# Kernel optimization log

Measured on AMD Instinct MI355X. Metric: run time of the kernel, lower is better.

The kernel has to match this reference:

```python
import jax, jax.numpy as jnp
import numpy as np
import math

PHI = (1.0 + math.sqrt(5.0)) / 2.0
LUT_N = 4096
_TWO_PI = 2.0 * math.pi
_ang = np.arange(LUT_N, dtype=np.float32) * (_TWO_PI / LUT_N)
SIN_T = jnp.asarray(np.sin(_ang), dtype=jnp.float32)
COS_T = jnp.asarray(np.cos(_ang), dtype=jnp.float32)


def lookup_sin_cos(theta):
    # Linearly-interpolated 4096-entry sin/cos LUT over [0, 2pi)
    pos = theta * (LUT_N / _TWO_PI)
    i0f = jnp.floor(pos)
    frac = pos - i0f
    i0 = i0f.astype(jnp.int32) % LUT_N
    i1 = (i0 + 1) % LUT_N
    sin = SIN_T[i0] * (1.0 - frac) + SIN_T[i1] * frac
    cos = COS_T[i0] * (1.0 - frac) + COS_T[i1] * frac
    return sin, cos


def setup_inputs() -> dict:
    key = jax.random.key(0)
    ks = jax.random.split(key, 10)
    B, D, H = 8192, 1024, 4
    dh = D // H
    return {
        "x_real": jax.random.normal(ks[0], (B, D), dtype=jnp.float32),
        "x_imag": jax.random.normal(ks[1], (B, D), dtype=jnp.float32),
        "t": jax.random.uniform(ks[2], (B,), dtype=jnp.float32) * 100.0,
        "trigger_real": jax.random.normal(ks[3], (H, dh), dtype=jnp.float32) * 0.5,
        "trigger_imag": jax.random.normal(ks[4], (H, dh), dtype=jnp.float32) * 0.5,
        "w_query": jax.random.normal(ks[5], (H, dh), dtype=jnp.float32) * 0.02,
        "b_query": jnp.zeros((H, dh), dtype=jnp.float32),
        "w_out": jax.random.normal(ks[6], (D,), dtype=jnp.float32) * 0.02,
        "b_out": jnp.zeros((D,), dtype=jnp.float32),
        "beta": jnp.abs(jax.random.normal(ks[7], (D,), dtype=jnp.float32)) * 5.0 + 5.0,
    }


def reference(x_real, x_imag, t, trigger_real, trigger_imag, w_query, b_query,
              w_out, b_out, beta):
    B, D = x_real.shape
    H, dh = trigger_real.shape
    t_phi = (t * PHI)[:, None]            # (B, 1)

    # ---- per-head conjugate interference ----
    xr = x_real.reshape(B, H, dh)
    xi = x_imag.reshape(B, H, dh)
    wl_q = 1.0 + jnp.abs(w_query)          # (H, dh)
    tp = t_phi[:, :, None]                 # (B, 1, 1)
    th_r = xr / wl_q + b_query + tp        # (B, H, dh)
    th_i = xi / wl_q + b_query + tp
    sin_r, cos_r = lookup_sin_cos(th_r)
    sin_i, cos_i = lookup_sin_cos(th_i)
    q_r = cos_r * cos_i - sin_r * sin_i
    q_i = cos_r * sin_i + sin_r * cos_i
    int_r = (q_r * trigger_real + q_i * trigger_imag).sum(-1)   # (B, H)
    int_i = (q_r * trigger_imag - q_i * trigger_real).sum(-1)   # (B, H)
    tot_r = int_r.mean(-1)                 # (B,)
    tot_i = int_i.mean(-1)
    mag = jnp.sqrt(tot_r * tot_r + tot_i * tot_i + 1e-8)[:, None]  # (B, 1)

    # ---- gated Q-EMA memory update (memory starts at zeros) ----
    beta_eff = 1.0 / (1.0 + jnp.abs(beta))     # (D,)
    w_eff = 1.0 / (1.0 + jnp.abs(w_out))       # (D,)
    decay = jnp.minimum(jnp.exp(-beta_eff * w_eff), 0.9999)
    write_scale = w_eff * (1.0 - decay)        # (D,)
    # initial memory is zero, so memory*decay term vanishes
    mem_r = x_real * mag * write_scale
    mem_i = x_imag * mag * write_scale

    # ---- Euler output projection ----
    wl_out = 1.0 + jnp.abs(w_out)
    to_r = mem_r / wl_out + b_out + t_phi
    to_i = mem_i / wl_out + b_out + t_phi
    s_or, c_or = lookup_sin_cos(to_r)
    s_oi, c_oi = lookup_sin_cos(to_i)
    out_real = c_or * c_oi - s_or * s_oi
    out_imag = c_or * s_oi + s_or * c_oi
    return out_real, out_imag
```

## Files before the change

kernel.cpp:

```cpp
#include <hip/hip_runtime.h>
#include <math.h>

#define DCOLS 1024
#define PHI_F 1.61803398874989484820f

__global__ __launch_bounds__(256) void echo_kernel(
    const float* __restrict__ x_real,
    const float* __restrict__ x_imag,
    const float* __restrict__ t,
    const float* __restrict__ trig_r,
    const float* __restrict__ trig_i,
    const float* __restrict__ w_query,
    const float* __restrict__ b_query,
    const float* __restrict__ w_out,
    const float* __restrict__ b_out,
    const float* __restrict__ beta,
    float* __restrict__ out_real,
    float* __restrict__ out_imag)
{
    const int b   = blockIdx.x;
    const int tid = threadIdx.x;
    const int d0  = tid << 2;
    const long base = (long)b * DCOLS + d0;

    const float tphi2 = 2.0f * PHI_F * t[b];

    float4 xr = *reinterpret_cast<const float4*>(x_real + base);
    float4 xi = *reinterpret_cast<const float4*>(x_imag + base);
    float4 wq = *reinterpret_cast<const float4*>(w_query + d0);
    float4 bq = *reinterpret_cast<const float4*>(b_query + d0);
    float4 tr = *reinterpret_cast<const float4*>(trig_r  + d0);
    float4 ti = *reinterpret_cast<const float4*>(trig_i  + d0);

    float s_sum[4];
    float tot_r = 0.f, tot_i = 0.f;
    #pragma unroll
    for (int k = 0; k < 4; ++k) {
        const float xrk = (&xr.x)[k], xik = (&xi.x)[k];
        const float s = xrk + xik;
        s_sum[k] = s;
        const float inv_wlq = __builtin_amdgcn_rcpf(1.0f + fabsf((&wq.x)[k]));
        const float ang = fmaf(s, inv_wlq, 2.0f * (&bq.x)[k] + tphi2);
        float sn, cs;
        __sincosf(ang, &sn, &cs);
        const float trk = (&tr.x)[k], tik = (&ti.x)[k];
        tot_r = fmaf(cs, trk, fmaf(sn, tik, tot_r));
        tot_i = fmaf(cs, tik, fmaf(-sn, trk, tot_i));
    }

    #pragma unroll
    for (int m = 32; m >= 1; m >>= 1) {
        tot_r += __shfl_xor(tot_r, m, 64);
        tot_i += __shfl_xor(tot_i, m, 64);
    }
    __shared__ float red_r[4], red_i[4];
    const int wid = tid >> 6;
    if ((tid & 63) == 0) { red_r[wid] = tot_r; red_i[wid] = tot_i; }
    __syncthreads();
    float TR = ((red_r[0] + red_r[1]) + (red_r[2] + red_r[3])) * 0.25f;
    float TI = ((red_i[0] + red_i[1]) + (red_i[2] + red_i[3])) * 0.25f;
    const float mag = sqrtf(fmaf(TR, TR, fmaf(TI, TI, 1e-8f)));

    float4 wo = *reinterpret_cast<const float4*>(w_out + d0);
    float4 bo = *reinterpret_cast<const float4*>(b_out + d0);
    float4 be = *reinterpret_cast<const float4*>(beta  + d0);

    float4 o_r, o_i;
    #pragma unroll
    for (int k = 0; k < 4; ++k) {
        const float weff = __builtin_amdgcn_rcpf(1.0f + fabsf((&wo.x)[k]));
        const float beff = __builtin_amdgcn_rcpf(1.0f + fabsf((&be.x)[k]));
        const float decay = fminf(__expf(-beff * weff), 0.9999f);
        const float wscale = weff * (1.0f - decay);
        const float ang = fmaf(s_sum[k], mag * wscale * weff,
                               2.0f * (&bo.x)[k] + tphi2);
        float sn, cs;
        __sincosf(ang, &sn, &cs);
        (&o_r.x)[k] = cs;
        (&o_i.x)[k] = sn;
    }
    *reinterpret_cast<float4*>(out_real + base) = o_r;
    *reinterpret_cast<float4*>(out_imag + base) = o_i;
}

extern "C" void kernel_launch(void* const* d_in, const int* in_sizes, int n_in,
                              void* d_out, int out_size, void* d_ws, size_t ws_size,
                              hipStream_t stream) {
    const float* x_real = (const float*)d_in[0];
    const float* x_imag = (const float*)d_in[1];
    const float* t      = (const float*)d_in[2];
    const float* trig_r = (const float*)d_in[3];
    const float* trig_i = (const float*)d_in[4];
    const float* w_q    = (const float*)d_in[5];
    const float* b_q    = (const float*)d_in[6];
    const float* w_out  = (const float*)d_in[7];
    const float* b_out  = (const float*)d_in[8];
    const float* beta   = (const float*)d_in[9];

    const int B = in_sizes[2];
    float* out_real = (float*)d_out;
    float* out_imag = (float*)d_out + (long)B * DCOLS;

    echo_kernel<<<B, 256, 0, stream>>>(x_real, x_imag, t,
                                       trig_r, trig_i, w_q, b_q,
                                       w_out, b_out, beta,
                                       out_real, out_imag);
}
```

Measured before the change: 141.5 us.

## Process one row per wave persistently with register-cached params and prefetch

Switches from one 256-thread block per row to one wavefront per row. Each wave loops over rows spaced total_waves apart and prefetches the next row's x and t while it computes the current one. Per-column parameters, including decay and write scale, are computed once per thread and kept in registers, which removes the shared-memory reduction, the __syncthreads, and the repeated parameter work. In exchange the kernel uses more registers (launch bounds 256,2) and launches fewer blocks (B/16 blocks, so each wave handles 4 rows), which may limit latency hiding.

```diff
diff --git a/kernel.cpp b/kernel.cpp
--- a/kernel.cpp
+++ b/kernel.cpp
@@ -4,83 +4,123 @@
 #define DCOLS 1024
 #define PHI_F 1.61803398874989484820f
 
-__global__ __launch_bounds__(256) void echo_kernel(
-    const float* __restrict__ x_real,
-    const float* __restrict__ x_imag,
+__global__ __launch_bounds__(256, 2) void echo_kernel(
+    const float* __restrict__ x_real, const float* __restrict__ x_imag,
     const float* __restrict__ t,
-    const float* __restrict__ trig_r,
-    const float* __restrict__ trig_i,
-    const float* __restrict__ w_query,
-    const float* __restrict__ b_query,
-    const float* __restrict__ w_out,
-    const float* __restrict__ b_out,
+    const float* __restrict__ trig_r, const float* __restrict__ trig_i,
+    const float* __restrict__ w_query, const float* __restrict__ b_query,
+    const float* __restrict__ w_out, const float* __restrict__ b_out,
     const float* __restrict__ beta,
-    float* __restrict__ out_real,
-    float* __restrict__ out_imag)
+    float* __restrict__ out_real, float* __restrict__ out_imag,
+    int B, int total_waves)
 {
-    const int b   = blockIdx.x;
-    const int tid = threadIdx.x;
-    const int d0  = tid << 2;
-    const long base = (long)b * DCOLS + d0;
+    const int tid  = threadIdx.x;
+    const int lane = tid & 63;
+    const int wid  = tid >> 6;
+    const int wave = (blockIdx.x << 2) + wid;
+    const int c0   = lane << 2;
 
-    const float tphi2 = 2.0f * PHI_F * t[b];
-
-    float4 xr = *reinterpret_cast<const float4*>(x_real + base);
-    float4 xi = *reinterpret_cast<const float4*>(x_imag + base);
-    float4 wq = *reinterpret_cast<const float4*>(w_query + d0);
-    float4 bq = *reinterpret_cast<const float4*>(b_query + d0);
-    float4 tr = *reinterpret_cast<const float4*>(trig_r  + d0);
-    float4 ti = *reinterpret_cast<const float4*>(trig_i  + d0);
-
-    float s_sum[4];
-    float tot_r = 0.f, tot_i = 0.f;
+    float invq[16], addq[16], trr[16], tri[16], c2[16], addo[16];
     #pragma unroll
     for (int k = 0; k < 4; ++k) {
-        const float xrk = (&xr.x)[k], xik = (&xi.x)[k];
-        const float s = xrk + xik;
-        s_sum[k] = s;
-        const float inv_wlq = __builtin_amdgcn_rcpf(1.0f + fabsf((&wq.x)[k]));
-        const float ang = fmaf(s, inv_wlq, 2.0f * (&bq.x)[k] + tphi2);
-        float sn, cs;
-        __sincosf(ang, &sn, &cs);
-        const float trk = (&tr.x)[k], tik = (&ti.x)[k];
-        tot_r = fmaf(cs, trk, fmaf(sn, tik, tot_r));
-        tot_i = fmaf(cs, tik, fmaf(-sn, trk, tot_i));
+        const int c = (k << 8) + c0;
+        const float4 wq = *reinterpret_cast<const float4*>(w_query + c);
+        const float4 bq = *reinterpret_cast<const float4*>(b_query + c);
+        const float4 tr = *reinterpret_cast<const float4*>(trig_r  + c);
+        const float4 ti = *reinterpret_cast<const float4*>(trig_i  + c);
+        const float4 wo = *reinterpret_cast<const float4*>(w_out   + c);
+        const float4 bo = *reinterpret_cast<const float4*>(b_out   + c);
+        const float4 be = *reinterpret_cast<const float4*>(beta    + c);
+        #pragma unroll
+        for (int j = 0; j < 4; ++j) {
+            const int e = (k << 2) + j;
+            invq[e] = __builtin_amdgcn_rcpf(1.0f + fabsf((&wq.x)[j]));
+            addq[e] = 2.0f * (&bq.x)[j];
+            trr[e]  = (&tr.x)[j];
+            tri[e]  = (&ti.x)[j];
+            const float weff  = __builtin_amdgcn_rcpf(1.0f + fabsf((&wo.x)[j]));
+            const float beff  = __builtin_amdgcn_rcpf(1.0f + fabsf((&be.x)[j]));
+            const float decay = fminf(__expf(-beff * weff), 0.9999f);
+            c2[e]   = weff * weff * (1.0f - decay);
+            addo[e] = 2.0f * (&bo.x)[j];
+        }
     }
 
-    #pragma unroll
-    for (int m = 32; m >= 1; m >>= 1) {
-        tot_r += __shfl_xor(tot_r, m, 64);
-        tot_i += __shfl_xor(tot_i, m, 64);
-    }
-    __shared__ float red_r[4], red_i[4];
-    const int wid = tid >> 6;
-    if ((tid & 63) == 0) { red_r[wid] = tot_r; red_i[wid] = tot_i; }
-    __syncthreads();
-    float TR = ((red_r[0] + red_r[1]) + (red_r[2] + red_r[3])) * 0.25f;
-    float TI = ((red_i[0] + red_i[1]) + (red_i[2] + red_i[3])) * 0.25f;
-    const float mag = sqrtf(fmaf(TR, TR, fmaf(TI, TI, 1e-8f)));
+    int row = wave;
+    if (row >= B) return;
+    long base = (long)row * DCOLS + c0;
 
-    float4 wo = *reinterpret_cast<const float4*>(w_out + d0);
-    float4 bo = *reinterpret_cast<const float4*>(b_out + d0);
-    float4 be = *reinterpret_cast<const float4*>(beta  + d0);
-
-    float4 o_r, o_i;
+    float4 xr[4], xi[4];
     #pragma unroll
     for (int k = 0; k < 4; ++k) {
-        const float weff = __builtin_amdgcn_rcpf(1.0f + fabsf((&wo.x)[k]));
-        const float beff = __builtin_amdgcn_rcpf(1.0f + fabsf((&be.x)[k]));
-        const float decay = fminf(__expf(-beff * weff), 0.9999f);
-        const float wscale = weff * (1.0f - decay);
-        const float ang = fmaf(s_sum[k], mag * wscale * weff,
-                               2.0f * (&bo.x)[k] + tphi2);
-        float sn, cs;
-        __sincosf(ang, &sn, &cs);
-        (&o_r.x)[k] = cs;
-        (&o_i.x)[k] = sn;
+        xr[k] = *reinterpret_cast<const float4*>(x_real + base + (k << 8));
+        xi[k] = *reinterpret_cast<const float4*>(x_imag + base + (k << 8));
     }
-    *reinterpret_cast<float4*>(out_real + base) = o_r;
-    *reinterpret_cast<float4*>(out_imag + base) = o_i;
+    float tcur = t[row];
+
+    while (true) {
+        const int  nrow = row + total_waves;
+        const bool more = (nrow < B);
+        const float tphi2 = 2.0f * PHI_F * tcur;
+
+        float s[16];
+        float tot_r = 0.f, tot_i = 0.f;
+        #pragma unroll
+        for (int k = 0; k < 4; ++k) {
+            #pragma unroll
+            for (int j = 0; j < 4; ++j) {
+                const int e = (k << 2) + j;
+                const float sv = (&xr[k].x)[j] + (&xi[k].x)[j];
+                s[e] = sv;
+                const float ang = fmaf(sv, invq[e], addq[e] + tphi2);
+                float sn, cs;
+                __sincosf(ang, &sn, &cs);
+                tot_r = fmaf(cs, trr[e], fmaf(sn, tri[e], tot_r));
+                tot_i = fmaf(cs, tri[e], fmaf(-sn, trr[e], tot_i));
+            }
+        }
+
+        float4 nxr[4], nxi[4];
+        float tnext = 0.f;
+        const long nbase = (long)nrow * DCOLS + c0;
+        if (more) {
+            #pragma unroll
+            for (int k = 0; k < 4; ++k) {
+                nxr[k] = *reinterpret_cast<const float4*>(x_real + nbase + (k << 8));
+                nxi[k] = *reinterpret_cast<const float4*>(x_imag + nbase + (k << 8));
+            }
+            tnext = t[nrow];
+        }
+
+        #pragma unroll
+        for (int m = 32; m >= 1; m >>= 1) {
+            tot_r += __shfl_xor(tot_r, m, 64);
+            tot_i += __shfl_xor(tot_i, m, 64);
+        }
+        const float TR = tot_r * 0.25f, TI = tot_i * 0.25f;
+        const float mag = sqrtf(fmaf(TR, TR, fmaf(TI, TI, 1e-8f)));
+
+        #pragma unroll
+        for (int k = 0; k < 4; ++k) {
+            float4 o_r, o_i;
+            #pragma unroll
+            for (int j = 0; j < 4; ++j) {
+                const int e = (k << 2) + j;
+                const float ang = fmaf(s[e], mag * c2[e], addo[e] + tphi2);
+                float sn, cs;
+                __sincosf(ang, &sn, &cs);
+                (&o_r.x)[j] = cs;
+                (&o_i.x)[j] = sn;
+            }
+            *reinterpret_cast<float4*>(out_real + base + (k << 8)) = o_r;
+            *reinterpret_cast<float4*>(out_imag + base + (k << 8)) = o_i;
+        }
+
+        if (!more) break;
+        row = nrow; base = nbase; tcur = tnext;
+        #pragma unroll
+        for (int k = 0; k < 4; ++k) { xr[k] = nxr[k]; xi[k] = nxi[k]; }
+    }
 }
 
 extern "C" void kernel_launch(void* const* d_in, const int* in_sizes, int n_in,
@@ -101,8 +141,12 @@
     float* out_real = (float*)d_out;
     float* out_imag = (float*)d_out + (long)B * DCOLS;
 
-    echo_kernel<<<B, 256, 0, stream>>>(x_real, x_imag, t,
-                                       trig_r, trig_i, w_q, b_q,
-                                       w_out, b_out, beta,
-                                       out_real, out_imag);
+    const int blocks = (B + 15) / 16;
+    const int total_waves = blocks * 4;
+
+    echo_kernel<<<blocks, 256, 0, stream>>>(x_real, x_imag, t,
+                                            trig_r, trig_i, w_q, b_q,
+                                            w_out, b_out, beta,
+                                            out_real, out_imag,
+                                            B, total_waves);
 }
```

After: 129.9 us. 8.2% less time.
